# Optimization experiments

Measured on AMD Instinct MI355X. Metric: run time of the kernel, lower is better.

## Reference

```python
import jax, jax.numpy as jnp
import numpy as np

N = 1048576   # total nodes in the graph batch
B = 16384     # number of graphs (segments)
D = 64        # candidate feature dim
EPS = 0.05    # eps_clip


def setup_inputs() -> dict:
    key = jax.random.key(0)
    k1, k2, k3 = jax.random.split(key, 3)
    candidates = jax.random.normal(k1, (N, D), dtype=jnp.float32)
    values = jax.random.normal(k2, (N,), dtype=jnp.float32)
    batch_idx = jnp.sort(jax.random.randint(k3, (N,), 0, B)).astype(jnp.int64)
    return {"candidates": candidates, "values": values, "batch_idx": batch_idx}


def reference(candidates, values, batch_idx):
    # --- batched_argmax ---
    ones = jnp.ones_like(values)
    cnt = jax.ops.segment_sum(ones, batch_idx, num_segments=B)[batch_idx]      # bincount + index_select
    vmax = jax.ops.segment_max(values, batch_idx, num_segments=B)[batch_idx]   # global_max_pool + index_select
    probs = (values == vmax).astype(values.dtype) + EPS / (cnt - 1.0)
    probs = jnp.where(jnp.isinf(probs), jnp.ones_like(probs), probs)           # isinf fix (count==1)
    # --- batched_sample: masked Categorical per segment == per-segment Gumbel-max ---
    g = jax.random.gumbel(jax.random.key(42), (N,), dtype=values.dtype)
    score = jnp.log(probs) + g
    smax = jax.ops.segment_max(score, batch_idx, num_segments=B)[batch_idx]
    node_ids = jnp.arange(N, dtype=jnp.int32)
    winner = jnp.where(score == smax, node_ids, -1)
    actions = jax.ops.segment_max(winner, batch_idx, num_segments=B)           # [B], sampled node per graph
    # torch.unique on sorted batch returns ascending ids; torch.flip reverses them,
    # so row i of the output corresponds to graph B-1-i.
    shifted_actions = actions[::-1]
    return candidates[shifted_actions]
```

## Files before the change

kernel.cpp:

```cpp
#include <hip/hip_runtime.h>


#define N_ELEMS 1048576
#define BSEG    16384
#define DDIM    64

#define GUMBEL_VARIANT 0

__device__ __forceinline__ unsigned rotl32(unsigned x, unsigned r) {
    return (x << r) | (x >> (32u - r));
}

#define TF_ROUND(r) { x0 += x1; x1 = rotl32(x1, (r)); x1 ^= x0; }

__device__ __forceinline__ void tf2x32(unsigned x0, unsigned x1,
                                       unsigned& o0, unsigned& o1) {
    const unsigned k0 = 0u, k1 = 42u;
    const unsigned ks2 = k0 ^ k1 ^ 0x1BD11BDAu;
    x0 += k0; x1 += k1;
    TF_ROUND(13) TF_ROUND(15) TF_ROUND(26) TF_ROUND(6)
    x0 += k1; x1 += ks2 + 1u;
    TF_ROUND(17) TF_ROUND(29) TF_ROUND(16) TF_ROUND(24)
    x0 += ks2; x1 += k0 + 2u;
    TF_ROUND(13) TF_ROUND(15) TF_ROUND(26) TF_ROUND(6)
    x0 += k0; x1 += k1 + 3u;
    TF_ROUND(17) TF_ROUND(29) TF_ROUND(16) TF_ROUND(24)
    x0 += k1; x1 += ks2 + 4u;
    TF_ROUND(13) TF_ROUND(15) TF_ROUND(26) TF_ROUND(6)
    x0 += ks2; x1 += k0 + 5u;
    o0 = x0; o1 = x1;
}

__device__ __forceinline__ unsigned gumbel_bits(unsigned i) {
    unsigned a, b;
    tf2x32(0u, i, a, b);
    return a ^ b;
}

__device__ __forceinline__ float gumbel_val(unsigned i) {
    unsigned bits = gumbel_bits(i);
    float f = __uint_as_float((bits >> 9) | 0x3f800000u) - 1.0f;
    const float tiny = 1.17549435e-38f;
    float u = fmaxf(tiny, f + tiny);
    return -logf(-logf(u));
}

__device__ __forceinline__ unsigned fenc(float f) {
    unsigned b = __float_as_uint(f);
    return (b & 0x80000000u) ? ~b : (b | 0x80000000u);
}
__device__ __forceinline__ float fdec(unsigned e) {
    unsigned b = (e & 0x80000000u) ? (e ^ 0x80000000u) : ~e;
    return __uint_as_float(b);
}

__global__ void k_stats(const float* __restrict__ vals,
                        const int* __restrict__ idx,
                        unsigned* __restrict__ cnt,
                        unsigned* __restrict__ vmax) {
    int i = blockIdx.x * 256 + threadIdx.x;
    int lane = threadIdx.x & 63;
    int b = idx[i];
    unsigned c = 1u;
    unsigned m = fenc(vals[i]);
#pragma unroll
    for (int d = 1; d < 64; d <<= 1) {
        int bo      = __shfl_up(b, d, 64);
        unsigned co = __shfl_up(c, d, 64);
        unsigned mo = __shfl_up(m, d, 64);
        if (lane >= d && bo == b) { c += co; m = (mo > m) ? mo : m; }
    }
    int bn = __shfl_down(b, 1, 64);
    if (lane == 63 || bn != b) {
        atomicAdd(&cnt[b], c);
        atomicMax(&vmax[b], m);
    }
}

__global__ void k_score(const float* __restrict__ vals,
                        const int* __restrict__ idx,
                        const unsigned* __restrict__ cnt,
                        const unsigned* __restrict__ vmax,
                        unsigned long long* __restrict__ packed) {
    int i = blockIdx.x * 256 + threadIdx.x;
    int lane = threadIdx.x & 63;
    int b = idx[i];
    float v = vals[i];
    float vm = fdec(vmax[b]);
    float c = (float)cnt[b];
    float probs = ((v == vm) ? 1.0f : 0.0f) + 0.05f / (c - 1.0f);
    if (isinf(probs)) probs = 1.0f;
    float score = logf(probs) + gumbel_val((unsigned)i);
    unsigned long long p =
        ((unsigned long long)fenc(score) << 32) | (unsigned long long)(unsigned)i;
#pragma unroll
    for (int d = 1; d < 64; d <<= 1) {
        int bo = __shfl_up(b, d, 64);
        unsigned long long po = __shfl_up(p, d, 64);
        if (lane >= d && bo == b) { p = (po > p) ? po : p; }
    }
    int bn = __shfl_down(b, 1, 64);
    if (lane == 63 || bn != b) atomicMax(&packed[b], p);
}

__global__ void k_gather(const float4* __restrict__ cand,
                         const unsigned long long* __restrict__ packed,
                         float4* __restrict__ out) {
    int t = blockIdx.x * 256 + threadIdx.x;
    int r = t >> 4;
    int q = t & 15;
    unsigned long long p = packed[BSEG - 1 - r];
    unsigned id = (unsigned)(p & 0xFFFFFFFFull);
    if (p == 0ull || id >= N_ELEMS) id = 0u;
    out[(size_t)r * 16 + q] = cand[(size_t)id * 16 + q];
}

extern "C" void kernel_launch(void* const* d_in, const int* in_sizes, int n_in,
                              void* d_out, int out_size, void* d_ws, size_t ws_size,
                              hipStream_t stream) {
    const float* cand = (const float*)d_in[0];
    const float* vals = (const float*)d_in[1];
    const int*   idx  = (const int*)d_in[2];
    float* out = (float*)d_out;

    unsigned long long* packed = (unsigned long long*)d_ws;
    unsigned* cnt  = (unsigned*)(packed + BSEG);
    unsigned* vmax = cnt + BSEG;

    hipMemsetAsync(d_ws, 0, (size_t)BSEG * 16, stream);

    k_stats <<<dim3(N_ELEMS / 256), dim3(256), 0, stream>>>(vals, idx, cnt, vmax);
    k_score <<<dim3(N_ELEMS / 256), dim3(256), 0, stream>>>(vals, idx, cnt, vmax, packed);
    k_gather<<<dim3(BSEG * 16 / 256), dim3(256), 0, stream>>>(
        (const float4*)cand, packed, (float4*)out);
}
```

Baseline: 312.4 us.

## Fuse three kernels into one persistent kernel with software grid barriers

Replaces the stats, score and gather launches with a single persistent kernel of 1024 blocks. Each thread handles four elements and keeps idx and vals in registers across phases, and the phases are separated by atomic-counter grid barriers. This removes two kernel launches and the second read of idx and vals. The barrier assumes every block is co-resident, and its spin guard can break out early and give wrong results if they are not.

```diff
diff --git a/kernel.cpp b/kernel.cpp
--- a/kernel.cpp
+++ b/kernel.cpp
@@ -3,9 +3,10 @@
 
 #define N_ELEMS 1048576
 #define BSEG    16384
-#define DDIM    64
-
-#define GUMBEL_VARIANT 0
+#define NB      1024
+#define NT      256
+#define CHUNK   (NB * NT)
+#define ITERS   (N_ELEMS / CHUNK)
 
 __device__ __forceinline__ unsigned rotl32(unsigned x, unsigned r) {
     return (x << r) | (x >> (32u - r));
@@ -31,14 +32,10 @@
     o0 = x0; o1 = x1;
 }
 
-__device__ __forceinline__ unsigned gumbel_bits(unsigned i) {
+__device__ __forceinline__ float gumbel_val(unsigned i) {
     unsigned a, b;
     tf2x32(0u, i, a, b);
-    return a ^ b;
-}
-
-__device__ __forceinline__ float gumbel_val(unsigned i) {
-    unsigned bits = gumbel_bits(i);
+    unsigned bits = a ^ b;
     float f = __uint_as_float((bits >> 9) | 0x3f800000u) - 1.0f;
     const float tiny = 1.17549435e-38f;
     float u = fmaxf(tiny, f + tiny);
@@ -54,83 +51,108 @@
     return __uint_as_float(b);
 }
 
-__global__ void k_stats(const float* __restrict__ vals,
-                        const int* __restrict__ idx,
-                        unsigned* __restrict__ cnt,
-                        unsigned* __restrict__ vmax) {
-    int i = blockIdx.x * 256 + threadIdx.x;
-    int lane = threadIdx.x & 63;
-    int b = idx[i];
-    unsigned c = 1u;
-    unsigned m = fenc(vals[i]);
-#pragma unroll
-    for (int d = 1; d < 64; d <<= 1) {
-        int bo      = __shfl_up(b, d, 64);
-        unsigned co = __shfl_up(c, d, 64);
-        unsigned mo = __shfl_up(m, d, 64);
-        if (lane >= d && bo == b) { c += co; m = (mo > m) ? mo : m; }
+__device__ __forceinline__ void grid_bar(unsigned* bar, int p) {
+    __syncthreads();
+    if (threadIdx.x == 0) {
+        __threadfence();
+        atomicAdd(bar, 1u);
+        const unsigned target = (unsigned)(NB * p);
+        int guard = 0;
+        while (__hip_atomic_load(bar, __ATOMIC_ACQUIRE,
+                                 __HIP_MEMORY_SCOPE_AGENT) < target) {
+            __builtin_amdgcn_s_sleep(2);
+            if (++guard > 200000) break;
+        }
+        __threadfence();
     }
-    int bn = __shfl_down(b, 1, 64);
-    if (lane == 63 || bn != b) {
-        atomicAdd(&cnt[b], c);
-        atomicMax(&vmax[b], m);
-    }
+    __syncthreads();
 }
 
-__global__ void k_score(const float* __restrict__ vals,
-                        const int* __restrict__ idx,
-                        const unsigned* __restrict__ cnt,
-                        const unsigned* __restrict__ vmax,
-                        unsigned long long* __restrict__ packed) {
-    int i = blockIdx.x * 256 + threadIdx.x;
-    int lane = threadIdx.x & 63;
-    int b = idx[i];
-    float v = vals[i];
-    float vm = fdec(vmax[b]);
-    float c = (float)cnt[b];
-    float probs = ((v == vm) ? 1.0f : 0.0f) + 0.05f / (c - 1.0f);
-    if (isinf(probs)) probs = 1.0f;
-    float score = logf(probs) + gumbel_val((unsigned)i);
-    unsigned long long p =
-        ((unsigned long long)fenc(score) << 32) | (unsigned long long)(unsigned)i;
+__global__ __launch_bounds__(NT, 4)
+void k_fused(const float4* __restrict__ cand,
+             const float*  __restrict__ vals,
+             const int*    __restrict__ idx,
+             float4*       __restrict__ out,
+             unsigned long long* __restrict__ packed,
+             unsigned*     __restrict__ cnt,
+             unsigned*     __restrict__ vmax,
+             unsigned*     __restrict__ bar) {
+    const int tid  = blockIdx.x * NT + threadIdx.x;
+    const int lane = threadIdx.x & 63;
+
+    int   bl[ITERS];
+    float vl[ITERS];
 #pragma unroll
-    for (int d = 1; d < 64; d <<= 1) {
-        int bo = __shfl_up(b, d, 64);
-        unsigned long long po = __shfl_up(p, d, 64);
-        if (lane >= d && bo == b) { p = (po > p) ? po : p; }
+    for (int it = 0; it < ITERS; ++it) {
+        const int i = it * CHUNK + tid;
+        const int   b = idx[i];
+        const float v = vals[i];
+        bl[it] = b; vl[it] = v;
+        unsigned c = 1u;
+        unsigned m = fenc(v);
+#pragma unroll
+        for (int d = 1; d < 64; d <<= 1) {
+            int      bo = __shfl_up(b, d, 64);
+            unsigned co = __shfl_up(c, d, 64);
+            unsigned mo = __shfl_up(m, d, 64);
+            if (lane >= d && bo == b) { c += co; if (mo > m) m = mo; }
+        }
+        const int bn = __shfl_down(b, 1, 64);
+        if (lane == 63 || bn != b) {
+            atomicAdd(&cnt[b], c);
+            atomicMax(&vmax[b], m);
+        }
     }
-    int bn = __shfl_down(b, 1, 64);
-    if (lane == 63 || bn != b) atomicMax(&packed[b], p);
-}
+    grid_bar(bar, 1);
 
-__global__ void k_gather(const float4* __restrict__ cand,
-                         const unsigned long long* __restrict__ packed,
-                         float4* __restrict__ out) {
-    int t = blockIdx.x * 256 + threadIdx.x;
-    int r = t >> 4;
-    int q = t & 15;
-    unsigned long long p = packed[BSEG - 1 - r];
-    unsigned id = (unsigned)(p & 0xFFFFFFFFull);
-    if (p == 0ull || id >= N_ELEMS) id = 0u;
-    out[(size_t)r * 16 + q] = cand[(size_t)id * 16 + q];
+#pragma unroll
+    for (int it = 0; it < ITERS; ++it) {
+        const int i = it * CHUNK + tid;
+        const int   b = bl[it];
+        const float v = vl[it];
+        const float vm = fdec(vmax[b]);
+        const float c  = (float)cnt[b];
+        float probs = ((v == vm) ? 1.0f : 0.0f) + 0.05f / (c - 1.0f);
+        if (isinf(probs)) probs = 1.0f;
+        const float score = logf(probs) + gumbel_val((unsigned)i);
+        unsigned long long p = ((unsigned long long)fenc(score) << 32)
+                             | (unsigned long long)(unsigned)i;
+#pragma unroll
+        for (int d = 1; d < 64; d <<= 1) {
+            int                bo = __shfl_up(b, d, 64);
+            unsigned long long po = __shfl_up(p, d, 64);
+            if (lane >= d && bo == b) { if (po > p) p = po; }
+        }
+        const int bn = __shfl_down(b, 1, 64);
+        if (lane == 63 || bn != b) atomicMax(&packed[b], p);
+    }
+    grid_bar(bar, 2);
+
+    {
+        const int r = tid >> 4;
+        const int q = tid & 15;
+        const unsigned long long p = packed[BSEG - 1 - r];
+        unsigned id = (unsigned)(p & 0xFFFFFFFFull);
+        if (p == 0ull || id >= N_ELEMS) id = 0u;
+        out[(size_t)r * 16 + q] = cand[(size_t)id * 16 + q];
+    }
 }
 
 extern "C" void kernel_launch(void* const* d_in, const int* in_sizes, int n_in,
                               void* d_out, int out_size, void* d_ws, size_t ws_size,
                               hipStream_t stream) {
-    const float* cand = (const float*)d_in[0];
-    const float* vals = (const float*)d_in[1];
-    const int*   idx  = (const int*)d_in[2];
-    float* out = (float*)d_out;
+    const float4* cand = (const float4*)d_in[0];
+    const float*  vals = (const float*)d_in[1];
+    const int*    idx  = (const int*)d_in[2];
+    float4* out = (float4*)d_out;
 
     unsigned long long* packed = (unsigned long long*)d_ws;
     unsigned* cnt  = (unsigned*)(packed + BSEG);
     unsigned* vmax = cnt + BSEG;
+    unsigned* bar  = vmax + BSEG;
 
-    hipMemsetAsync(d_ws, 0, (size_t)BSEG * 16, stream);
+    hipMemsetAsync(d_ws, 0, (size_t)BSEG * 16 + 64, stream);
 
-    k_stats <<<dim3(N_ELEMS / 256), dim3(256), 0, stream>>>(vals, idx, cnt, vmax);
-    k_score <<<dim3(N_ELEMS / 256), dim3(256), 0, stream>>>(vals, idx, cnt, vmax, packed);
-    k_gather<<<dim3(BSEG * 16 / 256), dim3(256), 0, stream>>>(
-        (const float4*)cand, packed, (float4*)out);
+    k_fused<<<dim3(NB), dim3(NT), 0, stream>>>(cand, vals, idx, out,
+                                               packed, cnt, vmax, bar);
 }
```

Measured after the change: 541.1 us. 73.2% more time.

## Fuse stats, scoring and gather into one wave-per-segment kernel with binary search

Applied to the files above, without the earlier changes.

Replaces the three kernels, the memset and the atomics with a single kernel where each wavefront owns one segment. Segment bounds come from a binary search over the sorted index array. The wave computes the max and the count directly, then the Gumbel scores, reduces to the argmax with wave shuffles, and gathers the chosen candidate row. This removes the second pass over values and indices, the global atomics and two extra launches, at the cost of about 40 dependent global loads per wave for the searches and partial wave utilisation on small segments.

```diff
diff --git a/kernel.cpp b/kernel.cpp
--- a/kernel.cpp
+++ b/kernel.cpp
@@ -4,8 +4,6 @@
 #define N_ELEMS 1048576
 #define BSEG    16384
 #define DDIM    64
-
-#define GUMBEL_VARIANT 0
 
 __device__ __forceinline__ unsigned rotl32(unsigned x, unsigned r) {
     return (x << r) | (x >> (32u - r));
@@ -31,14 +29,10 @@
     o0 = x0; o1 = x1;
 }
 
-__device__ __forceinline__ unsigned gumbel_bits(unsigned i) {
+__device__ __forceinline__ float gumbel_val(unsigned i) {
     unsigned a, b;
     tf2x32(0u, i, a, b);
-    return a ^ b;
-}
-
-__device__ __forceinline__ float gumbel_val(unsigned i) {
-    unsigned bits = gumbel_bits(i);
+    unsigned bits = a ^ b;
     float f = __uint_as_float((bits >> 9) | 0x3f800000u) - 1.0f;
     const float tiny = 1.17549435e-38f;
     float u = fmaxf(tiny, f + tiny);
@@ -49,88 +43,88 @@
     unsigned b = __float_as_uint(f);
     return (b & 0x80000000u) ? ~b : (b | 0x80000000u);
 }
-__device__ __forceinline__ float fdec(unsigned e) {
-    unsigned b = (e & 0x80000000u) ? (e ^ 0x80000000u) : ~e;
-    return __uint_as_float(b);
-}
 
-__global__ void k_stats(const float* __restrict__ vals,
-                        const int* __restrict__ idx,
-                        unsigned* __restrict__ cnt,
-                        unsigned* __restrict__ vmax) {
-    int i = blockIdx.x * 256 + threadIdx.x;
-    int lane = threadIdx.x & 63;
-    int b = idx[i];
-    unsigned c = 1u;
-    unsigned m = fenc(vals[i]);
+__global__ __launch_bounds__(256)
+void k_seg(const float4* __restrict__ cand,
+           const float*  __restrict__ vals,
+           const int*    __restrict__ idx,
+           float4*       __restrict__ out) {
+    const int wave = (blockIdx.x * 256 + threadIdx.x) >> 6;
+    const int lane = threadIdx.x & 63;
+    const int b    = wave;
+    if (wave >= BSEG) return;
+
+    int lo = 0, hi = N_ELEMS;
+    while (lo < hi) { int mid = (lo + hi) >> 1; if (idx[mid] < b) lo = mid + 1; else hi = mid; }
+    const int s_lo = lo;
+    hi = N_ELEMS;
+    while (lo < hi) { int mid = (lo + hi) >> 1; if (idx[mid] < b + 1) lo = mid + 1; else hi = mid; }
+    const int s_hi = lo;
+    const int n = s_hi - s_lo;
+
+    const int i0 = s_lo + lane;
+    const int i1 = s_lo + 64 + lane;
+    float v0 = 0.0f, v1 = 0.0f;
+    if (i0 < s_hi) v0 = vals[i0];
+    if (i1 < s_hi) v1 = vals[i1];
+
+    float m = -__builtin_inff();
+    if (i0 < s_hi) m = v0;
+    if (i1 < s_hi) m = fmaxf(m, v1);
+    for (int base = s_lo + 128; base < s_hi; base += 64) {
+        int i = base + lane;
+        if (i < s_hi) m = fmaxf(m, vals[i]);
+    }
+#pragma unroll
+    for (int d = 1; d < 64; d <<= 1) m = fmaxf(m, __shfl_xor(m, d, 64));
+
+    const float c = (float)n;
+    const float eps_term = 0.05f / (c - 1.0f);
+    unsigned long long p = 0ull;
+    if (i0 < s_hi) {
+        float probs = ((v0 == m) ? 1.0f : 0.0f) + eps_term;
+        if (isinf(probs)) probs = 1.0f;
+        float s = logf(probs) + gumbel_val((unsigned)i0);
+        p = ((unsigned long long)fenc(s) << 32) | (unsigned)i0;
+    }
+    if (i1 < s_hi) {
+        float probs = ((v1 == m) ? 1.0f : 0.0f) + eps_term;
+        if (isinf(probs)) probs = 1.0f;
+        float s = logf(probs) + gumbel_val((unsigned)i1);
+        unsigned long long q = ((unsigned long long)fenc(s) << 32) | (unsigned)i1;
+        if (q > p) p = q;
+    }
+    for (int base = s_lo + 128; base < s_hi; base += 64) {
+        int i = base + lane;
+        if (i < s_hi) {
+            float v = vals[i];
+            float probs = ((v == m) ? 1.0f : 0.0f) + eps_term;
+            if (isinf(probs)) probs = 1.0f;
+            float s = logf(probs) + gumbel_val((unsigned)i);
+            unsigned long long q = ((unsigned long long)fenc(s) << 32) | (unsigned)i;
+            if (q > p) p = q;
+        }
+    }
 #pragma unroll
     for (int d = 1; d < 64; d <<= 1) {
-        int bo      = __shfl_up(b, d, 64);
-        unsigned co = __shfl_up(c, d, 64);
-        unsigned mo = __shfl_up(m, d, 64);
-        if (lane >= d && bo == b) { c += co; m = (mo > m) ? mo : m; }
+        unsigned long long po = __shfl_xor(p, d, 64);
+        if (po > p) p = po;
     }
-    int bn = __shfl_down(b, 1, 64);
-    if (lane == 63 || bn != b) {
-        atomicAdd(&cnt[b], c);
-        atomicMax(&vmax[b], m);
-    }
-}
 
-__global__ void k_score(const float* __restrict__ vals,
-                        const int* __restrict__ idx,
-                        const unsigned* __restrict__ cnt,
-                        const unsigned* __restrict__ vmax,
-                        unsigned long long* __restrict__ packed) {
-    int i = blockIdx.x * 256 + threadIdx.x;
-    int lane = threadIdx.x & 63;
-    int b = idx[i];
-    float v = vals[i];
-    float vm = fdec(vmax[b]);
-    float c = (float)cnt[b];
-    float probs = ((v == vm) ? 1.0f : 0.0f) + 0.05f / (c - 1.0f);
-    if (isinf(probs)) probs = 1.0f;
-    float score = logf(probs) + gumbel_val((unsigned)i);
-    unsigned long long p =
-        ((unsigned long long)fenc(score) << 32) | (unsigned long long)(unsigned)i;
-#pragma unroll
-    for (int d = 1; d < 64; d <<= 1) {
-        int bo = __shfl_up(b, d, 64);
-        unsigned long long po = __shfl_up(p, d, 64);
-        if (lane >= d && bo == b) { p = (po > p) ? po : p; }
-    }
-    int bn = __shfl_down(b, 1, 64);
-    if (lane == 63 || bn != b) atomicMax(&packed[b], p);
-}
-
-__global__ void k_gather(const float4* __restrict__ cand,
-                         const unsigned long long* __restrict__ packed,
-                         float4* __restrict__ out) {
-    int t = blockIdx.x * 256 + threadIdx.x;
-    int r = t >> 4;
-    int q = t & 15;
-    unsigned long long p = packed[BSEG - 1 - r];
     unsigned id = (unsigned)(p & 0xFFFFFFFFull);
     if (p == 0ull || id >= N_ELEMS) id = 0u;
-    out[(size_t)r * 16 + q] = cand[(size_t)id * 16 + q];
+    const int r = BSEG - 1 - b;
+    if (lane < 16)
+        out[(size_t)r * 16 + lane] = cand[(size_t)id * 16 + lane];
 }
 
 extern "C" void kernel_launch(void* const* d_in, const int* in_sizes, int n_in,
                               void* d_out, int out_size, void* d_ws, size_t ws_size,
                               hipStream_t stream) {
-    const float* cand = (const float*)d_in[0];
-    const float* vals = (const float*)d_in[1];
-    const int*   idx  = (const int*)d_in[2];
-    float* out = (float*)d_out;
+    const float4* cand = (const float4*)d_in[0];
+    const float*  vals = (const float*)d_in[1];
+    const int*    idx  = (const int*)d_in[2];
+    float4* out = (float4*)d_out;
 
-    unsigned long long* packed = (unsigned long long*)d_ws;
-    unsigned* cnt  = (unsigned*)(packed + BSEG);
-    unsigned* vmax = cnt + BSEG;
-
-    hipMemsetAsync(d_ws, 0, (size_t)BSEG * 16, stream);
-
-    k_stats <<<dim3(N_ELEMS / 256), dim3(256), 0, stream>>>(vals, idx, cnt, vmax);
-    k_score <<<dim3(N_ELEMS / 256), dim3(256), 0, stream>>>(vals, idx, cnt, vmax, packed);
-    k_gather<<<dim3(BSEG * 16 / 256), dim3(256), 0, stream>>>(
-        (const float4*)cand, packed, (float4*)out);
+    k_seg<<<dim3(BSEG * 64 / 256), dim3(256), 0, stream>>>(cand, vals, idx, out);
 }
```

New measurement: 331.5 us. +6.1%, slower.
